# Optimization experiments

Hardware: AMD Instinct MI355X
Metric: run time of the kernel (lower is better)

Reference implementation:

```python
import jax, jax.numpy as jnp
import numpy as np

C = 64
CQK = C // 8  # query/key channels = 8


def setup_inputs() -> dict:
    key = jax.random.key(0)
    ks = jax.random.split(key, 7)
    B, D, H, W = 1, 16, 32, 32
    x = jax.random.normal(ks[0], (B, C, D, H, W), dtype=jnp.float32)
    # 1x1x1 Conv3d weights collapse to [out_ch, in_ch] matrices; std=0.01 per nn.init.normal_
    wq = 0.01 * jax.random.normal(ks[1], (CQK, C), dtype=jnp.float32)
    bq = jnp.zeros((CQK,), dtype=jnp.float32)
    wk = 0.01 * jax.random.normal(ks[2], (CQK, C), dtype=jnp.float32)
    bk = jnp.zeros((CQK,), dtype=jnp.float32)
    wv = 0.01 * jax.random.normal(ks[3], (C, C), dtype=jnp.float32)
    bv = jnp.zeros((C,), dtype=jnp.float32)
    gamma = jnp.zeros((1,), dtype=jnp.float32)  # nn.Parameter(torch.zeros(1))
    return {"x": x, "wq": wq, "bq": bq, "wk": wk, "bk": bk, "wv": wv, "bv": bv, "gamma": gamma}


def reference(x, wq, bq, wk, bk, wv, bv, gamma):
    B, Cc, D, H, W = x.shape
    N = D * H * W
    xf = x.reshape(B, Cc, N)  # [B, C, N]
    # 1x1x1 convs == per-position linear projections
    q = jnp.einsum('oc,bcn->bon', wq, xf) + bq[None, :, None]   # [B, CQK, N]
    k = jnp.einsum('oc,bcn->bon', wk, xf) + bk[None, :, None]   # [B, CQK, N]
    v = jnp.einsum('oc,bcn->bon', wv, xf) + bv[None, :, None]   # [B, C, N]
    # attention[b, i, j] = softmax_j( q[:, :, i] . k[:, :, j] )  -> [B, N, N]
    scores = jnp.einsum('bon,bom->bnm', q, k)
    attn = jax.nn.softmax(scores, axis=-1)
    # out[b, c, i] = sum_j v[b, c, j] * attn[b, i, j]
    out = jnp.einsum('bcm,bnm->bcn', v, attn).reshape(B, Cc, D, H, W)
    return x + gamma * out
```

## Files before the change

### kernel.cpp

```cpp
#include <hip/hip_runtime.h>

#define NPOS 16384
#define KSPLIT 8
#define KEYS_PER_BLK (NPOS / KSPLIT)
#define CHUNK 512
#define LOG2E 1.4426950408889634f

typedef short bf16x8 __attribute__((ext_vector_type(8)));
typedef unsigned short u16x8 __attribute__((ext_vector_type(8)));
typedef float floatx16 __attribute__((ext_vector_type(16)));
typedef float floatx2 __attribute__((ext_vector_type(2)));

static __device__ __forceinline__ unsigned short f2bf(float f) {
    return (unsigned short)(__builtin_bit_cast(unsigned int, f) >> 16);
}
static __device__ __forceinline__ float bf2f(unsigned short h) {
    return __builtin_bit_cast(float, (unsigned int)h << 16);
}

#if __has_builtin(__builtin_amdgcn_exp2f)
static __device__ __forceinline__ float exp2_fast(float x) {
    return __builtin_amdgcn_exp2f(x);
}
#else
static __device__ __forceinline__ float exp2_fast(float x) {
    float r;
    asm("v_exp_f32 %0, %1" : "=v"(r) : "v"(x));
    return r;
}
#endif

static __device__ __forceinline__ unsigned int pk_bf16(float e_even, float e_odd) {
    return __builtin_amdgcn_perm(__builtin_bit_cast(unsigned int, e_odd),
                                 __builtin_bit_cast(unsigned int, e_even),
                                 0x07060302u);
}

static __device__ __forceinline__ int sigma(int n) {
    const int w12 = n & 12;
    return (w12 == 4 || w12 == 8) ? (n ^ 12) : n;
}

__global__ __launch_bounds__(256) void proj_kernel(
    const float* __restrict__ x,
    const float* __restrict__ wq, const float* __restrict__ bq,
    const float* __restrict__ wk, const float* __restrict__ bk,
    const float* __restrict__ wv, const float* __restrict__ bv,
    unsigned short* __restrict__ qb16, unsigned short* __restrict__ kb16,
    unsigned short* __restrict__ vbg16)
{
    const int t = threadIdx.x;
    const int n = blockIdx.x * 256 + t;
    const int g = blockIdx.y;

    const float* w;
    const float* b;
    if (g == 0)      { w = wq; b = bq; }
    else if (g == 1) { w = wk; b = bk; }
    else             { w = wv + (g - 2) * 8 * 64; b = bv + (g - 2) * 8; }

    float acc[8];
#pragma unroll
    for (int oo = 0; oo < 8; ++oo) acc[oo] = b[oo];
#pragma unroll 16
    for (int c = 0; c < 64; ++c) {
        const float xv = x[c * NPOS + n];
#pragma unroll
        for (int oo = 0; oo < 8; ++oo)
            acc[oo] = fmaf(w[oo * 64 + c], xv, acc[oo]);
    }

    if (g == 0) {
        u16x8 qp;
#pragma unroll
        for (int j = 0; j < 8; ++j) qp[j] = f2bf(acc[j] * LOG2E);
        ((uint4*)qb16)[n] = __builtin_bit_cast(uint4, qp);
    } else if (g == 1) {
        u16x8 kp;
#pragma unroll
        for (int j = 0; j < 8; ++j) kp[j] = f2bf(acc[j]);
        ((uint4*)kb16)[n] = __builtin_bit_cast(uint4, kp);
    } else {
        const int o0 = (g - 2) * 8;
        const int np = sigma(n);
        const size_t base = (size_t)(np >> 3) * 512 + (np & 7);
#pragma unroll
        for (int oo = 0; oo < 8; ++oo)
            vbg16[base + (size_t)(o0 + oo) * 8] = f2bf(acc[oo]);
    }
}

static __device__ __forceinline__ void tile_pv(
    const floatx16& s, floatx2& den,
    const bf16x8* vf0, const bf16x8* vf1,
    floatx16& accA, floatx16& accB)
{
    float e[16];
#pragma unroll
    for (int r = 0; r < 16; ++r) e[r] = exp2_fast(s[r]);
#pragma unroll
    for (int p = 0; p < 8; ++p)
        den += (floatx2){e[2 * p], e[2 * p + 1]};
    unsigned int P[8];
#pragma unroll
    for (int p = 0; p < 8; ++p)
        P[p] = pk_bf16(e[2 * p], e[2 * p + 1]);
#pragma unroll
    for (int f = 0; f < 2; ++f) {
        uint4 afu;
        afu.x = P[4 * f + 0];
        afu.y = P[4 * f + 1];
        afu.z = P[4 * f + 2];
        afu.w = P[4 * f + 3];
        const bf16x8 af = __builtin_bit_cast(bf16x8, afu);
        __builtin_amdgcn_s_setprio(1);
        accA = __builtin_amdgcn_mfma_f32_32x32x16_bf16(af, vf0[f], accA, 0, 0, 0);
        accB = __builtin_amdgcn_mfma_f32_32x32x16_bf16(af, vf1[f], accB, 0, 0, 0);
        __builtin_amdgcn_s_setprio(0);
    }
}

__global__ __launch_bounds__(256, 4) void attn_kernel(
    const uint4* __restrict__ qb4,
    const uint4* __restrict__ kb4,
    const uint4* __restrict__ vbg4,
    unsigned short* __restrict__ nump,
    float* __restrict__ denp)
{
    __shared__ __align__(16) uint4 k_lds[512];

    const int t     = threadIdx.x;
    const int wave  = t >> 6;
    const int lane  = t & 63;
    const int m     = lane & 31;
    const int half  = lane >> 5;

    const int qblk = blockIdx.x >> 3;
    const int kq   = blockIdx.x & 7;
    const int i0   = qblk * 128;
    const int jb   = kq * KEYS_PER_BLK;
    const int qt   = (i0 >> 5) + wave;

    const uint4 zero4 = make_uint4(0, 0, 0, 0);
    const uint4 q4 = (half == 0) ? qb4[qt * 32 + m] : zero4;
    const bf16x8 bq = __builtin_bit_cast(bf16x8, q4);

    floatx16 accA = {}, accB = {};
    floatx2  den = {0.f, 0.f};

#pragma unroll 1
    for (int c4 = 0; c4 < 4; ++c4) {
        const int j0 = jb + c4 * CHUNK;

        bf16x8 vA0[2], vA1[2], vB0[2], vB1[2];
        {
            const int g8t = j0 >> 3;
#pragma unroll
            for (int f = 0; f < 2; ++f) {
                const int vidx = ((g8t + f * 2 + half) << 6) + m;
                vA0[f] = __builtin_bit_cast(bf16x8, vbg4[vidx]);
                vA1[f] = __builtin_bit_cast(bf16x8, vbg4[vidx + 32]);
            }
        }

        __syncthreads();
        k_lds[t]       = kb4[j0 + t];
        k_lds[256 + t] = kb4[j0 + 256 + t];
        __syncthreads();

#pragma unroll 1
        for (int st2 = 0; st2 < 8; ++st2) {
            const int stE = st2 * 2;
            {
                const bf16x8 ak =
                    __builtin_bit_cast(bf16x8, k_lds[stE * 32 + m]);
                const floatx16 s = __builtin_amdgcn_mfma_f32_32x32x16_bf16(
                    ak, bq, (floatx16){}, 0, 0, 0);
                const int g8o = (j0 + (stE + 1) * 32) >> 3;
#pragma unroll
                for (int f = 0; f < 2; ++f) {
                    const int vidx = ((g8o + f * 2 + half) << 6) + m;
                    vB0[f] = __builtin_bit_cast(bf16x8, vbg4[vidx]);
                    vB1[f] = __builtin_bit_cast(bf16x8, vbg4[vidx + 32]);
                }
                tile_pv(s, den, vA0, vA1, accA, accB);
            }
            {
                const bf16x8 ak =
                    __builtin_bit_cast(bf16x8, k_lds[(stE + 1) * 32 + m]);
                const floatx16 s = __builtin_amdgcn_mfma_f32_32x32x16_bf16(
                    ak, bq, (floatx16){}, 0, 0, 0);
                if (st2 < 7) {
                    const int g8e = (j0 + (stE + 2) * 32) >> 3;
#pragma unroll
                    for (int f = 0; f < 2; ++f) {
                        const int vidx = ((g8e + f * 2 + half) << 6) + m;
                        vA0[f] = __builtin_bit_cast(bf16x8, vbg4[vidx]);
                        vA1[f] = __builtin_bit_cast(bf16x8, vbg4[vidx + 32]);
                    }
                }
                tile_pv(s, den, vB0, vB1, accA, accB);
            }
        }
    }

    const float dl = den[0] + den[1];
    const float dw = dl + __shfl_xor(dl, 32);

    u16x8 o0, o1, o2, o3;
#pragma unroll
    for (int j = 0; j < 8; ++j) {
        o0[j] = f2bf(accA[j]);
        o1[j] = f2bf(accA[8 + j]);
        o2[j] = f2bf(accB[j]);
        o3[j] = f2bf(accB[8 + j]);
    }
    const size_t base = (((size_t)kq * 512 + qt) * 64 + lane) * 32;
    uint4* gdst = (uint4*)(nump + base);
    gdst[0] = __builtin_bit_cast(uint4, o0);
    gdst[1] = __builtin_bit_cast(uint4, o1);
    gdst[2] = __builtin_bit_cast(uint4, o2);
    gdst[3] = __builtin_bit_cast(uint4, o3);

    if (half == 0)
        denp[(size_t)kq * NPOS + qt * 32 + m] = dw;
}

__global__ __launch_bounds__(256) void finalize_kernel(
    const float* __restrict__ x,
    const unsigned short* __restrict__ nump,
    const float* __restrict__ denp,
    const float* __restrict__ gamma,
    float* __restrict__ out)
{
    const int b    = blockIdx.x;
    const int t    = threadIdx.x;
    const int lane = t >> 2;
    const int u    = t & 3;
    const int n0   = b * 32;

    __shared__ float dsum[32];
    __shared__ float ot[32 * 66];
    if (t < 32) dsum[t] = 0.f;
    __syncthreads();
    atomicAdd(&dsum[t & 31], denp[(size_t)(t >> 5) * NPOS + n0 + (t & 31)]);

    float ns[8];
#pragma unroll
    for (int j = 0; j < 8; ++j) ns[j] = 0.f;
#pragma unroll
    for (int kq = 0; kq < 8; ++kq) {
        const size_t base =
            (((size_t)kq * 512 + b) * 64 + lane) * 32 + u * 8;
        const u16x8 h = __builtin_bit_cast(u16x8, *(const uint4*)(nump + base));
#pragma unroll
        for (int j = 0; j < 8; ++j) ns[j] += bf2f(h[j]);
    }

    const int clow = lane & 31;
    const int hf   = lane >> 5;
#pragma unroll
    for (int j = 0; j < 8; ++j) {
        const int off = u * 8 + j;
        const int r   = off & 15;
        const int row = (r & 3) + 8 * (r >> 2) + 4 * hf;
        const int c   = (off >> 4) * 32 + clow;
        ot[row * 66 + c] = ns[j];
    }
    __syncthreads();

    const float g  = gamma[0];
    const int   c2 = t >> 2;
    const int   nq = t & 3;
#pragma unroll
    for (int j = 0; j < 8; ++j) {
        const int row = nq * 8 + j;
        const size_t gi = (size_t)c2 * NPOS + n0 + row;
        out[gi] = fmaf(g, ot[row * 66 + c2] *
                              __builtin_amdgcn_rcpf(dsum[row]), x[gi]);
    }
}

extern "C" void kernel_launch(void* const* d_in, const int* in_sizes, int n_in,
                              void* d_out, int out_size, void* d_ws, size_t ws_size,
                              hipStream_t stream)
{
    (void)in_sizes; (void)n_in; (void)out_size; (void)ws_size;

    const float* x     = (const float*)d_in[0];
    const float* wq    = (const float*)d_in[1];
    const float* bq    = (const float*)d_in[2];
    const float* wk    = (const float*)d_in[3];
    const float* bk    = (const float*)d_in[4];
    const float* wv    = (const float*)d_in[5];
    const float* bv    = (const float*)d_in[6];
    const float* gamma = (const float*)d_in[7];
    float* out = (float*)d_out;

    char* ws = (char*)d_ws;
    unsigned short* qb16  = (unsigned short*)(ws);
    unsigned short* kb16  = (unsigned short*)(ws + 262144);
    unsigned short* vbg16 = (unsigned short*)(ws + 524288);
    unsigned short* nump  = (unsigned short*)(ws + 2621440);
    float*          denp  = (float*)(ws + 19398656);

    proj_kernel<<<dim3(NPOS / 256, 10), 256, 0, stream>>>(
        x, wq, bq, wk, bk, wv, bv, qb16, kb16, vbg16);
    attn_kernel<<<(NPOS / 128) * KSPLIT, 256, 0, stream>>>(
        (const uint4*)qb16, (const uint4*)kb16, (const uint4*)vbg16,
        nump, denp);
    finalize_kernel<<<512, 256, 0, stream>>>(x, nump, denp, gamma, out);
}
```

Before: 137.0 us.

## Split key range across wave pairs with in-block LDS reduction, doubling grid

Each block now covers 64 queries instead of 128: two waves per query tile each process half of the keys in every chunk, and their partial numerators and denominators are combined through LDS at the end. The grid doubles, the V-register double-buffering software pipeline is removed in favour of simple per-step loads, s_setprio is dropped, and launch bounds target 6 blocks per CU. The aim is more parallelism and occupancy to hide memory latency, at the cost of an extra bf16 rounding in the partial sum and an extra reduction step with block syncs.

```diff
diff --git a/kernel.cpp b/kernel.cpp
--- a/kernel.cpp
+++ b/kernel.cpp
@@ -113,33 +113,34 @@
         afu.z = P[4 * f + 2];
         afu.w = P[4 * f + 3];
         const bf16x8 af = __builtin_bit_cast(bf16x8, afu);
-        __builtin_amdgcn_s_setprio(1);
         accA = __builtin_amdgcn_mfma_f32_32x32x16_bf16(af, vf0[f], accA, 0, 0, 0);
         accB = __builtin_amdgcn_mfma_f32_32x32x16_bf16(af, vf1[f], accB, 0, 0, 0);
-        __builtin_amdgcn_s_setprio(0);
-    }
-}
-
-__global__ __launch_bounds__(256, 4) void attn_kernel(
+    }
+}
+
+__global__ __launch_bounds__(256, 6) void attn_kernel(
     const uint4* __restrict__ qb4,
     const uint4* __restrict__ kb4,
     const uint4* __restrict__ vbg4,
     unsigned short* __restrict__ nump,
     float* __restrict__ denp)
 {
-    __shared__ __align__(16) uint4 k_lds[512];
+    __shared__ __align__(16) char smem[8704];
+    uint4* k_lds = (uint4*)smem;
 
     const int t     = threadIdx.x;
     const int wave  = t >> 6;
     const int lane  = t & 63;
     const int m     = lane & 31;
     const int half  = lane >> 5;
+    const int wtile = wave >> 1;
+    const int khalf = wave & 1;
 
     const int qblk = blockIdx.x >> 3;
     const int kq   = blockIdx.x & 7;
-    const int i0   = qblk * 128;
+    const int i0   = qblk * 64;
     const int jb   = kq * KEYS_PER_BLK;
-    const int qt   = (i0 >> 5) + wave;
+    const int qt   = (i0 >> 5) + wtile;
 
     const uint4 zero4 = make_uint4(0, 0, 0, 0);
     const uint4 q4 = (half == 0) ? qb4[qt * 32 + m] : zero4;
@@ -151,79 +152,81 @@
 #pragma unroll 1
     for (int c4 = 0; c4 < 4; ++c4) {
         const int j0 = jb + c4 * CHUNK;
-
-        bf16x8 vA0[2], vA1[2], vB0[2], vB1[2];
-        {
-            const int g8t = j0 >> 3;
-#pragma unroll
-            for (int f = 0; f < 2; ++f) {
-                const int vidx = ((g8t + f * 2 + half) << 6) + m;
-                vA0[f] = __builtin_bit_cast(bf16x8, vbg4[vidx]);
-                vA1[f] = __builtin_bit_cast(bf16x8, vbg4[vidx + 32]);
-            }
-        }
-
         __syncthreads();
         k_lds[t]       = kb4[j0 + t];
         k_lds[256 + t] = kb4[j0 + 256 + t];
         __syncthreads();
 
+        const int kwb = khalf * 256;
 #pragma unroll 1
-        for (int st2 = 0; st2 < 8; ++st2) {
-            const int stE = st2 * 2;
-            {
-                const bf16x8 ak =
-                    __builtin_bit_cast(bf16x8, k_lds[stE * 32 + m]);
-                const floatx16 s = __builtin_amdgcn_mfma_f32_32x32x16_bf16(
-                    ak, bq, (floatx16){}, 0, 0, 0);
-                const int g8o = (j0 + (stE + 1) * 32) >> 3;
-#pragma unroll
-                for (int f = 0; f < 2; ++f) {
-                    const int vidx = ((g8o + f * 2 + half) << 6) + m;
-                    vB0[f] = __builtin_bit_cast(bf16x8, vbg4[vidx]);
-                    vB1[f] = __builtin_bit_cast(bf16x8, vbg4[vidx + 32]);
-                }
-                tile_pv(s, den, vA0, vA1, accA, accB);
+        for (int st = 0; st < 8; ++st) {
+            const int kb_ = kwb + st * 32;
+            const bf16x8 ak = __builtin_bit_cast(bf16x8, k_lds[kb_ + m]);
+            const floatx16 s = __builtin_amdgcn_mfma_f32_32x32x16_bf16(
+                ak, bq, (floatx16){}, 0, 0, 0);
+
+            const int g8t = (j0 + kb_) >> 3;
+            bf16x8 vf0[2], vf1[2];
+#pragma unroll
+            for (int f = 0; f < 2; ++f) {
+                const int g8 = g8t + f * 2 + half;
+                vf0[f] = __builtin_bit_cast(bf16x8, vbg4[(size_t)g8 * 64 + m]);
+                vf1[f] = __builtin_bit_cast(bf16x8,
+                                            vbg4[(size_t)g8 * 64 + 32 + m]);
             }
-            {
-                const bf16x8 ak =
-                    __builtin_bit_cast(bf16x8, k_lds[(stE + 1) * 32 + m]);
-                const floatx16 s = __builtin_amdgcn_mfma_f32_32x32x16_bf16(
-                    ak, bq, (floatx16){}, 0, 0, 0);
-                if (st2 < 7) {
-                    const int g8e = (j0 + (stE + 2) * 32) >> 3;
-#pragma unroll
-                    for (int f = 0; f < 2; ++f) {
-                        const int vidx = ((g8e + f * 2 + half) << 6) + m;
-                        vA0[f] = __builtin_bit_cast(bf16x8, vbg4[vidx]);
-                        vA1[f] = __builtin_bit_cast(bf16x8, vbg4[vidx + 32]);
-                    }
-                }
-                tile_pv(s, den, vB0, vB1, accA, accB);
-            }
+
+            tile_pv(s, den, vf0, vf1, accA, accB);
         }
     }
 
     const float dl = den[0] + den[1];
     const float dw = dl + __shfl_xor(dl, 32);
 
-    u16x8 o0, o1, o2, o3;
-#pragma unroll
-    for (int j = 0; j < 8; ++j) {
-        o0[j] = f2bf(accA[j]);
-        o1[j] = f2bf(accA[8 + j]);
-        o2[j] = f2bf(accB[j]);
-        o3[j] = f2bf(accB[8 + j]);
-    }
-    const size_t base = (((size_t)kq * 512 + qt) * 64 + lane) * 32;
-    uint4* gdst = (uint4*)(nump + base);
-    gdst[0] = __builtin_bit_cast(uint4, o0);
-    gdst[1] = __builtin_bit_cast(uint4, o1);
-    gdst[2] = __builtin_bit_cast(uint4, o2);
-    gdst[3] = __builtin_bit_cast(uint4, o3);
-
-    if (half == 0)
-        denp[(size_t)kq * NPOS + qt * 32 + m] = dw;
+    __syncthreads();
+    float*          xden = (float*)smem;
+    unsigned short* xacc = (unsigned short*)(smem + 512);
+    if (khalf == 1) {
+        if (half == 0) xden[wtile * 32 + m] = dw;
+        u16x8 a0, a1, a2, a3;
+#pragma unroll
+        for (int j = 0; j < 8; ++j) {
+            a0[j] = f2bf(accA[j]);
+            a1[j] = f2bf(accA[8 + j]);
+            a2[j] = f2bf(accB[j]);
+            a3[j] = f2bf(accB[8 + j]);
+        }
+        uint4* dst = (uint4*)(xacc + ((size_t)wtile * 64 + lane) * 32);
+        dst[0] = __builtin_bit_cast(uint4, a0);
+        dst[1] = __builtin_bit_cast(uint4, a1);
+        dst[2] = __builtin_bit_cast(uint4, a2);
+        dst[3] = __builtin_bit_cast(uint4, a3);
+    }
+    __syncthreads();
+    if (khalf == 0) {
+        const uint4* src =
+            (const uint4*)(xacc + ((size_t)wtile * 64 + lane) * 32);
+        const u16x8 b0 = __builtin_bit_cast(u16x8, src[0]);
+        const u16x8 b1 = __builtin_bit_cast(u16x8, src[1]);
+        const u16x8 b2 = __builtin_bit_cast(u16x8, src[2]);
+        const u16x8 b3 = __builtin_bit_cast(u16x8, src[3]);
+        u16x8 o0, o1, o2, o3;
+#pragma unroll
+        for (int j = 0; j < 8; ++j) {
+            o0[j] = f2bf(accA[j]      + bf2f(b0[j]));
+            o1[j] = f2bf(accA[8 + j]  + bf2f(b1[j]));
+            o2[j] = f2bf(accB[j]      + bf2f(b2[j]));
+            o3[j] = f2bf(accB[8 + j]  + bf2f(b3[j]));
+        }
+        const size_t base = (((size_t)kq * 512 + qt) * 64 + lane) * 32;
+        uint4* gdst = (uint4*)(nump + base);
+        gdst[0] = __builtin_bit_cast(uint4, o0);
+        gdst[1] = __builtin_bit_cast(uint4, o1);
+        gdst[2] = __builtin_bit_cast(uint4, o2);
+        gdst[3] = __builtin_bit_cast(uint4, o3);
+
+        if (half == 0)
+            denp[(size_t)kq * NPOS + qt * 32 + m] = dw + xden[wtile * 32 + m];
+    }
 }
 
 __global__ __launch_bounds__(256) void finalize_kernel(
@@ -306,7 +309,7 @@
 
     proj_kernel<<<dim3(NPOS / 256, 10), 256, 0, stream>>>(
         x, wq, bq, wk, bk, wv, bv, qb16, kb16, vbg16);
-    attn_kernel<<<(NPOS / 128) * KSPLIT, 256, 0, stream>>>(
+    attn_kernel<<<(NPOS / 64) * KSPLIT, 256, 0, stream>>>(
         (const uint4*)qb16, (const uint4*)kb16, (const uint4*)vbg16,
         nump, denp);
     finalize_kernel<<<512, 256, 0, stream>>>(x, nump, denp, gamma, out);
```

Measured after the change: 151.1 us. +10.3%, slower.
